# Performance work log

Hardware: AMD Instinct MI355X
Metric: run time of the kernel (lower is better)

## Reference

```python
import jax, jax.numpy as jnp
import numpy as np

EPS = 1e-12  # matches torch F.normalize eps

def _l2norm(v, axis):
    return v / jnp.clip(jnp.linalg.norm(v, axis=axis, keepdims=True), EPS)

def setup_inputs() -> dict:
    key = jax.random.key(0)
    ks = jax.random.split(key, 5)
    B, D, H, W, K, OUT = 8, 512, 40, 40, 64, 4096
    x = jax.random.normal(ks[0], (B, D, H, W), dtype=jnp.float32)
    conv_w = jax.random.normal(ks[1], (K, D), dtype=jnp.float32) * (1.0 / np.sqrt(D))
    centers = jax.random.normal(ks[2], (D, K), dtype=jnp.float32)
    whiten_w = jax.random.normal(ks[3], (OUT, D * K), dtype=jnp.float32) * (1.0 / np.sqrt(D * K))
    whiten_b = jax.random.normal(ks[4], (OUT,), dtype=jnp.float32) * 0.01
    return {"x": x, "conv_w": conv_w, "centers": centers,
            "whiten_w": whiten_w, "whiten_b": whiten_b}

def reference(x, conv_w, centers, whiten_w, whiten_b):
    B, D = x.shape[0], x.shape[1]
    feat = x.reshape(B, D, -1)                       # [B, D, N]
    scores = jnp.einsum('kd,bdn->bkn', conv_w, feat)  # 1x1 Conv1d, no bias
    assign = jax.nn.softmax(scores, axis=1)           # softmax over clusters
    # vlad[b,d,k] = sum_n assign[b,k,n] * (feat[b,d,n] - centers[d,k])
    #            = (assign @ feat^T)[b,k,d]^T - (sum_n assign[b,k,n]) * centers[d,k]
    vlad = (jnp.einsum('bkn,bdn->bdk', assign, feat)
            - assign.sum(axis=-1)[:, None, :] * centers[None, :, :])  # [B, D, K]
    vlad = _l2norm(vlad, axis=1)                      # intra-normalization over D
    desc = vlad.reshape(B, -1)                        # [B, D*K]
    desc = _l2norm(desc, axis=1)
    desc = desc @ whiten_w.T + whiten_b               # whiten Linear -> [B, 4096]
    desc = _l2norm(desc, axis=1)
    return desc
```

## Files before the change

### kernel.cpp

```cpp
#include <hip/hip_runtime.h>

#define BB 8
#define DD 512
#define NPIX 1600
#define KK 64
#define OUTN 4096
#define DKN 32768

__global__ __launch_bounds__(256) void k1_scores(
    const float* __restrict__ x, const float* __restrict__ convw,
    float* __restrict__ assignT, float* __restrict__ asum) {
  __shared__ float cws[64 * 68];
  __shared__ float xs[64 * 68];
  int t = threadIdx.x;
  int b = blockIdx.y;
  int n0 = blockIdx.x * 64;
  int tn = t & 15, tk = t >> 4;
  int r = t >> 2, c = (t & 3) * 16;
  float acc[4][4] = {};

  for (int d0 = 0; d0 < DD; d0 += 64) {
    const float* cw = convw + (long)r * DD + d0 + c;
    const float* xp = x + ((long)(b * DD + d0 + r)) * NPIX + n0 + c;
#pragma unroll
    for (int q = 0; q < 4; q++) {
      *(float4*)(&cws[r * 68 + c + q * 4]) = *(const float4*)(cw + q * 4);
      *(float4*)(&xs[r * 68 + c + q * 4]) = *(const float4*)(xp + q * 4);
    }
    __syncthreads();
#pragma unroll 4
    for (int dd = 0; dd < 64; ++dd) {
      float a0 = cws[(tk * 4 + 0) * 68 + dd];
      float a1 = cws[(tk * 4 + 1) * 68 + dd];
      float a2 = cws[(tk * 4 + 2) * 68 + dd];
      float a3 = cws[(tk * 4 + 3) * 68 + dd];
      float4 bv = *(const float4*)(&xs[dd * 68 + tn * 4]);
      acc[0][0] += a0 * bv.x; acc[0][1] += a0 * bv.y; acc[0][2] += a0 * bv.z; acc[0][3] += a0 * bv.w;
      acc[1][0] += a1 * bv.x; acc[1][1] += a1 * bv.y; acc[1][2] += a1 * bv.z; acc[1][3] += a1 * bv.w;
      acc[2][0] += a2 * bv.x; acc[2][1] += a2 * bv.y; acc[2][2] += a2 * bv.z; acc[2][3] += a2 * bv.w;
      acc[3][0] += a3 * bv.x; acc[3][1] += a3 * bv.y; acc[3][2] += a3 * bv.z; acc[3][3] += a3 * bv.w;
    }
    __syncthreads();
  }

#pragma unroll
  for (int i = 0; i < 4; i++)
#pragma unroll
    for (int j = 0; j < 4; j++)
      cws[(tn * 4 + j) * 68 + tk * 4 + i] = acc[i][j];
  __syncthreads();

  if (t < 64) {
    int n = t;
    float vv[64];
    float m = -1e30f;
#pragma unroll
    for (int k2 = 0; k2 < 64; k2++) {
      float s = cws[n * 68 + k2];
      vv[k2] = s;
      m = fmaxf(m, s);
    }
    float ssum = 0.f;
#pragma unroll
    for (int k2 = 0; k2 < 64; k2++) {
      float e = expf(vv[k2] - m);
      vv[k2] = e;
      ssum += e;
    }
    float inv = 1.0f / ssum;
    float* ap = assignT + ((long)b * NPIX + n0 + n) * KK;
#pragma unroll
    for (int k2 = 0; k2 < 64; k2 += 4) {
      float4 o;
      o.x = vv[k2 + 0] * inv; o.y = vv[k2 + 1] * inv;
      o.z = vv[k2 + 2] * inv; o.w = vv[k2 + 3] * inv;
      *(float4*)(ap + k2) = o;
      cws[n * 68 + k2 + 0] = o.x; cws[n * 68 + k2 + 1] = o.y;
      cws[n * 68 + k2 + 2] = o.z; cws[n * 68 + k2 + 3] = o.w;
    }
  }
  __syncthreads();
  if (t < 64) {
    int k2 = t;
    float s = 0.f;
#pragma unroll 8
    for (int nn = 0; nn < 64; nn++) s += cws[nn * 68 + k2];
    atomicAdd(&asum[b * KK + k2], s);
  }
}

__global__ __launch_bounds__(256) void k2_vlad(
    const float* __restrict__ x, const float* __restrict__ assignT,
    float* __restrict__ vlad_part) {
  __shared__ float xs[64 * 68];
  __shared__ float as_[64 * 68];
  int t = threadIdx.x;
  int dt = blockIdx.x, ns = blockIdx.y, b = blockIdx.z;
  int d0 = dt * 64;
  int tk = t & 15, td = t >> 4;
  int r = t >> 2, c = (t & 3) * 16;
  float acc[4][4] = {};

  for (int nc = 0; nc < 320; nc += 64) {
    int n0 = ns * 320 + nc;
    const float* xp = x + ((long)(b * DD + d0 + r)) * NPIX + n0 + c;
    const float* ap = assignT + ((long)b * NPIX + n0 + r) * KK + c;
#pragma unroll
    for (int q = 0; q < 4; q++) {
      *(float4*)(&xs[r * 68 + c + q * 4]) = *(const float4*)(xp + q * 4);
      *(float4*)(&as_[r * 68 + c + q * 4]) = *(const float4*)(ap + q * 4);
    }
    __syncthreads();
#pragma unroll 4
    for (int nn = 0; nn < 64; ++nn) {
      float a0 = xs[(td * 4 + 0) * 68 + nn];
      float a1 = xs[(td * 4 + 1) * 68 + nn];
      float a2 = xs[(td * 4 + 2) * 68 + nn];
      float a3 = xs[(td * 4 + 3) * 68 + nn];
      float4 bv = *(const float4*)(&as_[nn * 68 + tk * 4]);
      acc[0][0] += a0 * bv.x; acc[0][1] += a0 * bv.y; acc[0][2] += a0 * bv.z; acc[0][3] += a0 * bv.w;
      acc[1][0] += a1 * bv.x; acc[1][1] += a1 * bv.y; acc[1][2] += a1 * bv.z; acc[1][3] += a1 * bv.w;
      acc[2][0] += a2 * bv.x; acc[2][1] += a2 * bv.y; acc[2][2] += a2 * bv.z; acc[2][3] += a2 * bv.w;
      acc[3][0] += a3 * bv.x; acc[3][1] += a3 * bv.y; acc[3][2] += a3 * bv.z; acc[3][3] += a3 * bv.w;
    }
    __syncthreads();
  }
  float* vp = vlad_part + (((long)ns * BB + b) * DD + d0) * KK;
#pragma unroll
  for (int i = 0; i < 4; i++) {
    float4 o = {acc[i][0], acc[i][1], acc[i][2], acc[i][3]};
    *(float4*)(vp + (td * 4 + i) * KK + tk * 4) = o;
  }
}

__global__ __launch_bounds__(256) void k3_norm(
    const float* __restrict__ vlad_part, const float* __restrict__ asum,
    const float* __restrict__ centers, float* __restrict__ desc,
    float* __restrict__ gsq) {
  __shared__ float sred[4];
  int k = blockIdx.x, b = blockIdx.y;
  int t = threadIdx.x;
  float a = asum[b * KK + k];
  float v[2];
#pragma unroll
  for (int h = 0; h < 2; h++) {
    int d = t + h * 256;
    float s = 0.f;
#pragma unroll
    for (int p = 0; p < 5; p++)
      s += vlad_part[(((long)p * BB + b) * DD + d) * KK + k];
    s -= a * centers[(long)d * KK + k];
    v[h] = s;
  }
  float ss = v[0] * v[0] + v[1] * v[1];
  for (int off = 32; off > 0; off >>= 1) ss += __shfl_down(ss, off, 64);
  if ((t & 63) == 0) sred[t >> 6] = ss;
  __syncthreads();
  float tot = sred[0] + sred[1] + sred[2] + sred[3];
  float sc = 1.0f / fmaxf(sqrtf(tot), 1e-12f);
#pragma unroll
  for (int h = 0; h < 2; h++) {
    int d = t + h * 256;
    desc[(long)b * DKN + (long)d * KK + k] = v[h] * sc;
  }
  if (t == 0) atomicAdd(&gsq[b], tot * sc * sc);
}

__global__ __launch_bounds__(256) void k4_whiten(
    const float* __restrict__ desc, const float* __restrict__ W,
    float* __restrict__ ydot) {
  int t = threadIdx.x;
  long o0 = (long)blockIdx.x * 8;
  float acc[8][8];
#pragma unroll
  for (int oo = 0; oo < 8; oo++)
#pragma unroll
    for (int bb = 0; bb < 8; bb++) acc[oo][bb] = 0.f;

  const float* wbase = W + o0 * DKN;
  for (int jt = 0; jt < DKN; jt += 1024) {
    int j = jt + t * 4;
    float4 d4[8];
#pragma unroll
    for (int bb = 0; bb < 8; bb++)
      d4[bb] = *(const float4*)(desc + (long)bb * DKN + j);
#pragma unroll
    for (int oo = 0; oo < 8; oo++) {
      float4 w4 = *(const float4*)(wbase + (long)oo * DKN + j);
#pragma unroll
      for (int bb = 0; bb < 8; bb++) {
        acc[oo][bb] += w4.x * d4[bb].x + w4.y * d4[bb].y +
                       w4.z * d4[bb].z + w4.w * d4[bb].w;
      }
    }
  }
  int lane = t & 63;
#pragma unroll
  for (int oo = 0; oo < 8; oo++)
#pragma unroll
    for (int bb = 0; bb < 8; bb++) {
      float v = acc[oo][bb];
      for (int off = 32; off > 0; off >>= 1) v += __shfl_down(v, off, 64);
      if (lane == 0) atomicAdd(&ydot[(long)bb * OUTN + o0 + oo], v);
    }
}

__global__ __launch_bounds__(256) void k5_final(
    const float* __restrict__ ydot, const float* __restrict__ gsq,
    const float* __restrict__ bias, float* __restrict__ out) {
  __shared__ float sred[4];
  int b = blockIdx.x, t = threadIdx.x;
  float g = fmaxf(sqrtf(gsq[b]), 1e-12f);
  float inv_g = 1.0f / g;
  float v[16];
  float ss = 0.f;
#pragma unroll
  for (int i = 0; i < 16; i++) {
    int o = t + i * 256;
    float val = ydot[(long)b * OUTN + o] * inv_g + bias[o];
    v[i] = val;
    ss += val * val;
  }
  for (int off = 32; off > 0; off >>= 1) ss += __shfl_down(ss, off, 64);
  if ((t & 63) == 0) sred[t >> 6] = ss;
  __syncthreads();
  float tot = sred[0] + sred[1] + sred[2] + sred[3];
  float sc = 1.0f / fmaxf(sqrtf(tot), 1e-12f);
#pragma unroll
  for (int i = 0; i < 16; i++) {
    int o = t + i * 256;
    out[(long)b * OUTN + o] = v[i] * sc;
  }
}

extern "C" void kernel_launch(void* const* d_in, const int* in_sizes, int n_in,
                              void* d_out, int out_size, void* d_ws,
                              size_t ws_size, hipStream_t stream) {
  const float* x = (const float*)d_in[0];
  const float* convw = (const float*)d_in[1];
  const float* centers = (const float*)d_in[2];
  const float* ww = (const float*)d_in[3];
  const float* wb = (const float*)d_in[4];
  float* out = (float*)d_out;

  float* base = (float*)d_ws;
  float* ydot = base;
  float* asum = base + 32768;
  float* gsq = base + 33280;
  float* assignT = base + 33288;
  float* desc = assignT;
  float* vlad_part = base + 33288 + 819200;

  hipMemsetAsync(base, 0, 33288 * sizeof(float), stream);

  hipLaunchKernelGGL(k1_scores, dim3(25, 8), dim3(256), 0, stream, x, convw,
                     assignT, asum);
  hipLaunchKernelGGL(k2_vlad, dim3(8, 5, 8), dim3(256), 0, stream, x, assignT,
                     vlad_part);
  hipLaunchKernelGGL(k3_norm, dim3(64, 8), dim3(256), 0, stream, vlad_part,
                     asum, centers, desc, gsq);
  hipLaunchKernelGGL(k4_whiten, dim3(512), dim3(256), 0, stream, desc, ww,
                     ydot);
  hipLaunchKernelGGL(k5_final, dim3(8), dim3(256), 0, stream, ydot, gsq, wb,
                     out);
}
```

Measured before the change: 830.8 us.

## Parallelize softmax, split VLAD over more pixel chunks, split whitening reduction

The softmax in k1 now uses all 256 threads, four per pixel, with shuffle reductions for max and sum. Previously only 64 threads did this work. k2 now launches 25 pixel splits of 64 instead of 5 splits of 320, which gives far more blocks. It writes partials in a k-major transposed layout so k3 reads them coalesced along d. k4 splits the 32768-long reduction into two halves across a second grid dimension to double block count; this relies on the epilogue accumulating into the zeroed ydot, and k3 must now sum five times more partials.

```diff
diff --git a/kernel.cpp b/kernel.cpp
--- a/kernel.cpp
+++ b/kernel.cpp
@@ -6,6 +6,7 @@
 #define KK 64
 #define OUTN 4096
 #define DKN 32768
+#define NSPLIT 25
 
 __global__ __launch_bounds__(256) void k1_scores(
     const float* __restrict__ x, const float* __restrict__ convw,
@@ -50,91 +51,92 @@
       cws[(tn * 4 + j) * 68 + tk * 4 + i] = acc[i][j];
   __syncthreads();
 
-  if (t < 64) {
-    int n = t;
-    float vv[64];
+  {
+    int n = t >> 2;
+    int kq = (t & 3) * 16;
+    float v[16];
     float m = -1e30f;
 #pragma unroll
-    for (int k2 = 0; k2 < 64; k2++) {
-      float s = cws[n * 68 + k2];
-      vv[k2] = s;
-      m = fmaxf(m, s);
-    }
+    for (int q = 0; q < 4; q++) {
+      float4 s4 = *(const float4*)(&cws[n * 68 + kq + q * 4]);
+      v[q * 4 + 0] = s4.x; v[q * 4 + 1] = s4.y;
+      v[q * 4 + 2] = s4.z; v[q * 4 + 3] = s4.w;
+      m = fmaxf(m, fmaxf(fmaxf(s4.x, s4.y), fmaxf(s4.z, s4.w)));
+    }
+    m = fmaxf(m, __shfl_xor(m, 1, 64));
+    m = fmaxf(m, __shfl_xor(m, 2, 64));
     float ssum = 0.f;
 #pragma unroll
-    for (int k2 = 0; k2 < 64; k2++) {
-      float e = expf(vv[k2] - m);
-      vv[k2] = e;
-      ssum += e;
-    }
+    for (int i = 0; i < 16; i++) {
+      v[i] = expf(v[i] - m);
+      ssum += v[i];
+    }
+    ssum += __shfl_xor(ssum, 1, 64);
+    ssum += __shfl_xor(ssum, 2, 64);
     float inv = 1.0f / ssum;
-    float* ap = assignT + ((long)b * NPIX + n0 + n) * KK;
-#pragma unroll
-    for (int k2 = 0; k2 < 64; k2 += 4) {
+    float* ap = assignT + ((long)b * NPIX + n0 + n) * KK + kq;
+#pragma unroll
+    for (int q = 0; q < 4; q++) {
       float4 o;
-      o.x = vv[k2 + 0] * inv; o.y = vv[k2 + 1] * inv;
-      o.z = vv[k2 + 2] * inv; o.w = vv[k2 + 3] * inv;
-      *(float4*)(ap + k2) = o;
-      cws[n * 68 + k2 + 0] = o.x; cws[n * 68 + k2 + 1] = o.y;
-      cws[n * 68 + k2 + 2] = o.z; cws[n * 68 + k2 + 3] = o.w;
-    }
-  }
-  __syncthreads();
-  if (t < 64) {
-    int k2 = t;
+      o.x = v[q * 4 + 0] * inv; o.y = v[q * 4 + 1] * inv;
+      o.z = v[q * 4 + 2] * inv; o.w = v[q * 4 + 3] * inv;
+      *(float4*)(ap + q * 4) = o;
+      *(float4*)(&cws[n * 68 + kq + q * 4]) = o;
+    }
+  }
+  __syncthreads();
+  {
+    int k2i = t & 63, ng = t >> 6;
     float s = 0.f;
-#pragma unroll 8
-    for (int nn = 0; nn < 64; nn++) s += cws[nn * 68 + k2];
-    atomicAdd(&asum[b * KK + k2], s);
+#pragma unroll
+    for (int nn = ng * 16; nn < ng * 16 + 16; nn++) s += cws[nn * 68 + k2i];
+    atomicAdd(&asum[b * KK + k2i], s);
   }
 }
 
 __global__ __launch_bounds__(256) void k2_vlad(
     const float* __restrict__ x, const float* __restrict__ assignT,
-    float* __restrict__ vlad_part) {
+    float* __restrict__ vpT) {
   __shared__ float xs[64 * 68];
   __shared__ float as_[64 * 68];
   int t = threadIdx.x;
   int dt = blockIdx.x, ns = blockIdx.y, b = blockIdx.z;
-  int d0 = dt * 64;
+  int d0 = dt * 64, n0 = ns * 64;
   int tk = t & 15, td = t >> 4;
   int r = t >> 2, c = (t & 3) * 16;
   float acc[4][4] = {};
 
-  for (int nc = 0; nc < 320; nc += 64) {
-    int n0 = ns * 320 + nc;
-    const float* xp = x + ((long)(b * DD + d0 + r)) * NPIX + n0 + c;
-    const float* ap = assignT + ((long)b * NPIX + n0 + r) * KK + c;
-#pragma unroll
-    for (int q = 0; q < 4; q++) {
-      *(float4*)(&xs[r * 68 + c + q * 4]) = *(const float4*)(xp + q * 4);
-      *(float4*)(&as_[r * 68 + c + q * 4]) = *(const float4*)(ap + q * 4);
-    }
-    __syncthreads();
+  const float* xp = x + ((long)(b * DD + d0 + r)) * NPIX + n0 + c;
+  const float* ap = assignT + ((long)b * NPIX + n0 + r) * KK + c;
+#pragma unroll
+  for (int q = 0; q < 4; q++) {
+    *(float4*)(&xs[r * 68 + c + q * 4]) = *(const float4*)(xp + q * 4);
+    *(float4*)(&as_[r * 68 + c + q * 4]) = *(const float4*)(ap + q * 4);
+  }
+  __syncthreads();
 #pragma unroll 4
-    for (int nn = 0; nn < 64; ++nn) {
-      float a0 = xs[(td * 4 + 0) * 68 + nn];
-      float a1 = xs[(td * 4 + 1) * 68 + nn];
-      float a2 = xs[(td * 4 + 2) * 68 + nn];
-      float a3 = xs[(td * 4 + 3) * 68 + nn];
-      float4 bv = *(const float4*)(&as_[nn * 68 + tk * 4]);
-      acc[0][0] += a0 * bv.x; acc[0][1] += a0 * bv.y; acc[0][2] += a0 * bv.z; acc[0][3] += a0 * bv.w;
-      acc[1][0] += a1 * bv.x; acc[1][1] += a1 * bv.y; acc[1][2] += a1 * bv.z; acc[1][3] += a1 * bv.w;
-      acc[2][0] += a2 * bv.x; acc[2][1] += a2 * bv.y; acc[2][2] += a2 * bv.z; acc[2][3] += a2 * bv.w;
-      acc[3][0] += a3 * bv.x; acc[3][1] += a3 * bv.y; acc[3][2] += a3 * bv.z; acc[3][3] += a3 * bv.w;
-    }
-    __syncthreads();
-  }
-  float* vp = vlad_part + (((long)ns * BB + b) * DD + d0) * KK;
-#pragma unroll
-  for (int i = 0; i < 4; i++) {
-    float4 o = {acc[i][0], acc[i][1], acc[i][2], acc[i][3]};
-    *(float4*)(vp + (td * 4 + i) * KK + tk * 4) = o;
+  for (int nn = 0; nn < 64; ++nn) {
+    float a0 = xs[(td * 4 + 0) * 68 + nn];
+    float a1 = xs[(td * 4 + 1) * 68 + nn];
+    float a2 = xs[(td * 4 + 2) * 68 + nn];
+    float a3 = xs[(td * 4 + 3) * 68 + nn];
+    float4 bv = *(const float4*)(&as_[nn * 68 + tk * 4]);
+    acc[0][0] += a0 * bv.x; acc[0][1] += a0 * bv.y; acc[0][2] += a0 * bv.z; acc[0][3] += a0 * bv.w;
+    acc[1][0] += a1 * bv.x; acc[1][1] += a1 * bv.y; acc[1][2] += a1 * bv.z; acc[1][3] += a1 * bv.w;
+    acc[2][0] += a2 * bv.x; acc[2][1] += a2 * bv.y; acc[2][2] += a2 * bv.z; acc[2][3] += a2 * bv.w;
+    acc[3][0] += a3 * bv.x; acc[3][1] += a3 * bv.y; acc[3][2] += a3 * bv.z; acc[3][3] += a3 * bv.w;
+  }
+  float* vp = vpT + (((long)ns * BB + b) * KK) * DD;
+#pragma unroll
+  for (int j = 0; j < 4; j++) {
+    int k = tk * 4 + j;
+    float4 o = {acc[0][j], acc[1][j], acc[2][j], acc[3][j]};
+    *(float4*)(vp + (long)k * DD + d0 + td * 4) = o;
   }
 }
 
 __global__ __launch_bounds__(256) void k3_norm(
-    const float* __restrict__ vlad_part, const float* __restrict__ asum,
+    const float* __restrict__ vpT, const float* __restrict__ asum,
     const float* __restrict__ centers, float* __restrict__ desc,
     float* __restrict__ gsq) {
   __shared__ float sred[4];
@@ -146,9 +148,9 @@
   for (int h = 0; h < 2; h++) {
     int d = t + h * 256;
     float s = 0.f;
-#pragma unroll
-    for (int p = 0; p < 5; p++)
-      s += vlad_part[(((long)p * BB + b) * DD + d) * KK + k];
+#pragma unroll 5
+    for (int p = 0; p < NSPLIT; p++)
+      s += vpT[(((long)p * BB + b) * KK + k) * DD + d];
     s -= a * centers[(long)d * KK + k];
     v[h] = s;
   }
@@ -171,6 +173,7 @@
     float* __restrict__ ydot) {
   int t = threadIdx.x;
   long o0 = (long)blockIdx.x * 8;
+  int jbase = blockIdx.y * (DKN / 2);
   float acc[8][8];
 #pragma unroll
   for (int oo = 0; oo < 8; oo++)
@@ -178,8 +181,8 @@
     for (int bb = 0; bb < 8; bb++) acc[oo][bb] = 0.f;
 
   const float* wbase = W + o0 * DKN;
-  for (int jt = 0; jt < DKN; jt += 1024) {
-    int j = jt + t * 4;
+  for (int jt = 0; jt < DKN / 2; jt += 1024) {
+    int j = jbase + jt + t * 4;
     float4 d4[8];
 #pragma unroll
     for (int bb = 0; bb < 8; bb++)
@@ -249,17 +252,17 @@
   float* gsq = base + 33280;
   float* assignT = base + 33288;
   float* desc = assignT;
-  float* vlad_part = base + 33288 + 819200;
+  float* vpT = base + 33288 + 819200;
 
   hipMemsetAsync(base, 0, 33288 * sizeof(float), stream);
 
   hipLaunchKernelGGL(k1_scores, dim3(25, 8), dim3(256), 0, stream, x, convw,
                      assignT, asum);
-  hipLaunchKernelGGL(k2_vlad, dim3(8, 5, 8), dim3(256), 0, stream, x, assignT,
-                     vlad_part);
-  hipLaunchKernelGGL(k3_norm, dim3(64, 8), dim3(256), 0, stream, vlad_part,
-                     asum, centers, desc, gsq);
-  hipLaunchKernelGGL(k4_whiten, dim3(512), dim3(256), 0, stream, desc, ww,
+  hipLaunchKernelGGL(k2_vlad, dim3(8, NSPLIT, 8), dim3(256), 0, stream, x,
+                     assignT, vpT);
+  hipLaunchKernelGGL(k3_norm, dim3(64, 8), dim3(256), 0, stream, vpT, asum,
+                     centers, desc, gsq);
+  hipLaunchKernelGGL(k4_whiten, dim3(512, 2), dim3(256), 0, stream, desc, ww,
                      ydot);
   hipLaunchKernelGGL(k5_final, dim3(8), dim3(256), 0, stream, ydot, gsq, wb,
                      out);
```

After: 801.3 us. -3.5%, faster.
